# Kernel tuning notes

Measured on AMD Instinct MI355X. Metric: run time of the kernel, lower is better.

Reference implementation:

```python
import jax, jax.numpy as jnp
import numpy as np

# Config matching init_kwargs: in_dim=128, kernal_sz=8 -> d=16 units per side
D = 16      # grid of units per side
K = 8       # kernel (patch) size
C = 3       # input channels
OUT = 1000  # out_chnls (codebook size per unit)
B = 64      # batch
BETA = 10.0 # softmax temperature (init arg beta)


def setup_inputs() -> dict:
    key = jax.random.key(0)
    k1, k2 = jax.random.split(key)
    x = jax.random.normal(k1, (B, C, D * K, D * K), dtype=jnp.float32)
    # Independent weights per (w,h) unit: [d, d, out_chnls, k*k*C]
    W = jax.random.normal(k2, (D, D, OUT, C * K * K), dtype=jnp.float32) * 0.02
    return {"x": x, "W": W}


def reference(x, W):
    Bn = x.shape[0]
    P = C * K * K
    # Patch extraction matching x[:, :, k*w:k*w+k, k*h:k*h+k].reshape(B, -1)
    # (channel-major flatten of each non-overlapping k x k patch)
    patches = (
        x.reshape(Bn, C, D, K, D, K)          # (b, c, w, kh, h, kw)
         .transpose(0, 2, 4, 1, 3, 5)          # (b, w, h, c, kh, kw)
         .reshape(Bn, D, D, P)
    )
    # infer: per-unit linear infer_step -> a[b, o, w, h]
    a = jnp.einsum('bwhp,whop->bowh', patches, W)
    # per-patch competitive softmax selection over the unit's channels
    z = jax.nn.softmax(BETA * a, axis=1)
    # predict: decode code back to patch via W^T, scatter back into image
    pred = jnp.einsum('bowh,whop->bwhp', z, W)
    p = (
        pred.reshape(Bn, D, D, C, K, K)        # (b, w, h, c, kh, kw)
            .transpose(0, 3, 1, 4, 2, 5)        # (b, c, w, kh, h, kw)
            .reshape(Bn, C, D * K, D * K)
    )
    return p
```

## Files before the change

### kernel.cpp

```cpp
#include <hip/hip_runtime.h>


#define Dd 16
#define OUTC 1000
#define Pp 192
#define Bb 64
#define OT 64
#define NT 16
#define THREADS 512
#define BETA 10.0f

typedef __attribute__((ext_vector_type(8))) short short8;
typedef __attribute__((ext_vector_type(4))) float f32x4;

#define MFMA(a, b, c) __builtin_amdgcn_mfma_f32_16x16x32_bf16((a), (b), (c), 0, 0, 0)

__device__ __forceinline__ unsigned f2bf(float f) {
  unsigned u = __float_as_uint(f);
  return (u + 0x7fffu + ((u >> 16) & 1u)) >> 16;
}

__device__ __forceinline__ int paddr(int b, int p) {
  return b * 384 + ((((p) >> 3) ^ (b & 7)) << 4) + ((p) & 7) * 2;
}
__device__ __forceinline__ int waddr(int o, int p) {
  int f = (o & 7) ^ ((o >> 3) & 3);
  return o * 384 + ((((p) >> 3) ^ f) << 4) + ((p) & 7) * 2;
}
__device__ __forceinline__ int eaddr(int b, int o) {
  return b * 128 + ((((o) >> 3) ^ (b & 7)) << 4) + ((o) & 7) * 2;
}

__device__ __forceinline__ void cvt_hilo4(const float4 v, uint2& hi2, uint2& lo2) {
  unsigned h0 = f2bf(v.x), h1 = f2bf(v.y), h2 = f2bf(v.z), h3 = f2bf(v.w);
  float l0 = v.x - __uint_as_float(h0 << 16);
  float l1 = v.y - __uint_as_float(h1 << 16);
  float l2 = v.z - __uint_as_float(h2 << 16);
  float l3 = v.w - __uint_as_float(h3 << 16);
  unsigned g0 = f2bf(l0), g1 = f2bf(l1), g2 = f2bf(l2), g3 = f2bf(l3);
  hi2 = make_uint2(h0 | (h1 << 16), h2 | (h3 << 16));
  lo2 = make_uint2(g0 | (g1 << 16), g2 | (g3 << 16));
}

__global__ __launch_bounds__(THREADS, 2)
void local_layer_mfma(const float* __restrict__ x,
                      const float* __restrict__ W,
                      float* __restrict__ out) {
  __shared__ unsigned short pH[Bb * Pp];
  __shared__ unsigned short pL[Bb * Pp];
  __shared__ unsigned short wHs[OT * Pp];
  __shared__ unsigned short wLs[OT * Pp];
  __shared__ unsigned short eSs[Bb * OT];
  __shared__ float lS[Bb];

  char* pHc = (char*)pH; char* pLc = (char*)pL;
  char* wHc = (char*)wHs; char* wLc = (char*)wLs;
  char* eSc = (char*)eSs;

  const int u = blockIdx.x, uw = u >> 4, uh = u & 15;
  const int tid = threadIdx.x;
  const int wv = tid >> 6, lane = tid & 63;
  const int lr = lane & 15, lg = lane >> 4;
  const int mw = wv & 1;
  const int ow = wv >> 1;
  const int bB = 32 * mw;

  const float* Wu = W + (size_t)u * (OUTC * Pp);

  if (tid < Bb) lS[tid] = 0.f;

  float4 R[6];
#pragma unroll
  for (int k = 0; k < 6; ++k) {
    int i4 = tid + THREADS * k;
    int o = i4 / 48, p = (i4 % 48) * 4;
    R[k] = *reinterpret_cast<const float4*>(Wu + o * Pp + p);
  }

  for (int i4 = tid; i4 < Bb * 48; i4 += THREADS) {
    int b = i4 / 48, q = i4 - b * 48, p = q * 4;
    int c = p >> 6, kh = (p >> 3) & 7, kw = p & 7;
    float4 v = *reinterpret_cast<const float4*>(
        x + ((size_t)((b * 3 + c) * 128 + uw * 8 + kh) * 128 + uh * 8 + kw));
    uint2 hi2, lo2;
    cvt_hilo4(v, hi2, lo2);
    *reinterpret_cast<uint2*>(pHc + paddr(b, p)) = hi2;
    *reinterpret_cast<uint2*>(pLc + paddr(b, p)) = lo2;
  }

#pragma unroll
  for (int k = 0; k < 6; ++k) {
    int i4 = tid + THREADS * k;
    int o = i4 / 48, p = (i4 % 48) * 4;
    uint2 hi2, lo2;
    cvt_hilo4(R[k], hi2, lo2);
    *reinterpret_cast<uint2*>(wHc + waddr(o, p)) = hi2;
    *reinterpret_cast<uint2*>(wLc + waddr(o, p)) = lo2;
  }
  __syncthreads();

  short8 pa_h[2][6], pa_l[2][6];
#pragma unroll
  for (int h = 0; h < 2; ++h)
#pragma unroll
    for (int ks = 0; ks < 6; ++ks) {
      pa_h[h][ks] = *reinterpret_cast<const short8*>(pHc + paddr(bB + 16 * h + lr, 32 * ks + 8 * lg));
      pa_l[h][ks] = *reinterpret_cast<const short8*>(pLc + paddr(bB + 16 * h + lr, 32 * ks + 8 * lg));
    }

  f32x4 pacc[2][3];
#pragma unroll
  for (int h = 0; h < 2; ++h)
#pragma unroll
    for (int f = 0; f < 3; ++f) pacc[h][f] = (f32x4){0.f, 0.f, 0.f, 0.f};
  float lPartA[2][4] = {{0.f, 0.f, 0.f, 0.f}, {0.f, 0.f, 0.f, 0.f}};

  for (int t = 0; t < NT; ++t) {
    if (t + 1 < NT) {
#pragma unroll
      for (int k = 0; k < 6; ++k) {
        int i4 = tid + THREADS * k;
        int o = i4 / 48, p = (i4 % 48) * 4;
        int o_g = (t + 1) * OT + o;
        R[k] = (o_g < OUTC)
                   ? *reinterpret_cast<const float4*>(Wu + (size_t)o_g * Pp + p)
                   : make_float4(0.f, 0.f, 0.f, 0.f);
      }
    }

    f32x4 acc[2] = {(f32x4){0.f, 0.f, 0.f, 0.f}, (f32x4){0.f, 0.f, 0.f, 0.f}};
#pragma unroll
    for (int ks = 0; ks < 6; ++ks) {
      short8 wbh = *reinterpret_cast<const short8*>(wHc + waddr(16 * ow + lr, 32 * ks + 8 * lg));
      short8 wbl = *reinterpret_cast<const short8*>(wLc + waddr(16 * ow + lr, 32 * ks + 8 * lg));
#pragma unroll
      for (int h = 0; h < 2; ++h) {
        acc[h] = MFMA(pa_h[h][ks], wbh, acc[h]);
        acc[h] = MFMA(pa_h[h][ks], wbl, acc[h]);
        acc[h] = MFMA(pa_l[h][ks], wbh, acc[h]);
      }
    }

    {
      const int o_g = t * OT + 16 * ow + lr;
      const bool valid = (o_g < OUTC);
#pragma unroll
      for (int h = 0; h < 2; ++h)
#pragma unroll
        for (int j = 0; j < 4; ++j) {
          float e = valid ? __expf(BETA * acc[h][j]) : 0.f;
          lPartA[h][j] += e;
          *reinterpret_cast<unsigned short*>(
              eSc + eaddr(bB + 16 * h + 4 * lg + j, 16 * ow + lr)) =
              (unsigned short)f2bf(e);
        }
    }
    __syncthreads();

    short8 ea[2][2];
#pragma unroll
    for (int h = 0; h < 2; ++h)
#pragma unroll
      for (int ks2 = 0; ks2 < 2; ++ks2)
        ea[h][ks2] = *reinterpret_cast<const short8*>(
            eSc + eaddr(bB + 16 * h + lr, 32 * ks2 + 8 * lg));

#pragma unroll
    for (int f = 0; f < 3; ++f) {
      const int p = 48 * ow + 16 * f + lr;
#pragma unroll
      for (int ks2 = 0; ks2 < 2; ++ks2) {
        short8 wb;
#pragma unroll
        for (int e8 = 0; e8 < 8; ++e8)
          wb[e8] = *reinterpret_cast<const short*>(
              wHc + waddr(32 * ks2 + 8 * lg + e8, p));
#pragma unroll
        for (int h = 0; h < 2; ++h)
          pacc[h][f] = MFMA(ea[h][ks2], wb, pacc[h][f]);
      }
    }
    __syncthreads();

    if (t + 1 < NT) {
#pragma unroll
      for (int k = 0; k < 6; ++k) {
        int i4 = tid + THREADS * k;
        int o = i4 / 48, p = (i4 % 48) * 4;
        uint2 hi2, lo2;
        cvt_hilo4(R[k], hi2, lo2);
        *reinterpret_cast<uint2*>(wHc + waddr(o, p)) = hi2;
        *reinterpret_cast<uint2*>(wLc + waddr(o, p)) = lo2;
      }
      __syncthreads();
    }
  }

#pragma unroll
  for (int h = 0; h < 2; ++h)
#pragma unroll
    for (int j = 0; j < 4; ++j) {
      float v = lPartA[h][j];
      v += __shfl_xor(v, 1, 16);
      v += __shfl_xor(v, 2, 16);
      v += __shfl_xor(v, 4, 16);
      v += __shfl_xor(v, 8, 16);
      if (lr == 0) atomicAdd(&lS[bB + 16 * h + 4 * lg + j], v);
    }
  __syncthreads();

#pragma unroll
  for (int h = 0; h < 2; ++h) {
    float inv[4];
#pragma unroll
    for (int j = 0; j < 4; ++j) inv[j] = 1.f / lS[bB + 16 * h + 4 * lg + j];
#pragma unroll
    for (int f = 0; f < 3; ++f) {
      const int p = 48 * ow + 16 * f + lr;
      const int c = p >> 6, kh = (p >> 3) & 7, kw = p & 7;
#pragma unroll
      for (int j = 0; j < 4; ++j) {
        const int b = bB + 16 * h + 4 * lg + j;
        out[((size_t)((b * 3 + c) * 128 + uw * 8 + kh)) * 128 + uh * 8 + kw] =
            pacc[h][f][j] * inv[j];
      }
    }
  }
}

extern "C" void kernel_launch(void* const* d_in, const int* in_sizes, int n_in,
                              void* d_out, int out_size, void* d_ws, size_t ws_size,
                              hipStream_t stream) {
  const float* x = (const float*)d_in[0];
  const float* W = (const float*)d_in[1];
  float* out = (float*)d_out;
  hipLaunchKernelGGL(local_layer_mfma, dim3(Dd * Dd), dim3(THREADS), 0, stream,
                     x, W, out);
}
```

Baseline: 292.5 us.

## Double block threads to sixteen waves and double-buffer weight tiles in LDS

Raises the block to 1024 threads so each wave computes 16 batch rows instead of 32, halving per-wave register state and fetching three float4 of W per thread per tile instead of six. The weight tile is now double-buffered in LDS, so the next tile is converted into the other buffer and one barrier per iteration is removed. Low-half patch fragments are now reread from LDS each iteration instead of being kept in registers. In exchange, LDS use grows to about 150KB per block and the B-operand weight fragments are read by twice as many waves.

```diff
diff --git a/kernel.cpp b/kernel.cpp
--- a/kernel.cpp
+++ b/kernel.cpp
@@ -7,7 +7,7 @@
 #define Bb 64
 #define OT 64
 #define NT 16
-#define THREADS 512
+#define THREADS 1024
 #define BETA 10.0f
 
 typedef __attribute__((ext_vector_type(8))) short short8;
@@ -42,43 +42,44 @@
   lo2 = make_uint2(g0 | (g1 << 16), g2 | (g3 << 16));
 }
 
-__global__ __launch_bounds__(THREADS, 2)
-void local_layer_mfma(const float* __restrict__ x,
-                      const float* __restrict__ W,
-                      float* __restrict__ out) {
+__global__ __launch_bounds__(THREADS, 4)
+void local_layer_mfma2(const float* __restrict__ x,
+                       const float* __restrict__ W,
+                       float* __restrict__ out) {
   __shared__ unsigned short pH[Bb * Pp];
   __shared__ unsigned short pL[Bb * Pp];
-  __shared__ unsigned short wHs[OT * Pp];
-  __shared__ unsigned short wLs[OT * Pp];
+  __shared__ unsigned short wH2[2][OT * Pp];
+  __shared__ unsigned short wL2[2][OT * Pp];
   __shared__ unsigned short eSs[Bb * OT];
   __shared__ float lS[Bb];
 
   char* pHc = (char*)pH; char* pLc = (char*)pL;
-  char* wHc = (char*)wHs; char* wLc = (char*)wLs;
   char* eSc = (char*)eSs;
 
   const int u = blockIdx.x, uw = u >> 4, uh = u & 15;
   const int tid = threadIdx.x;
   const int wv = tid >> 6, lane = tid & 63;
   const int lr = lane & 15, lg = lane >> 4;
-  const int mw = wv & 1;
-  const int ow = wv >> 1;
-  const int bB = 32 * mw;
+  const int mq = wv & 3;
+  const int ow = wv >> 2;
+  const int bB = 16 * mq;
 
   const float* Wu = W + (size_t)u * (OUTC * Pp);
 
   if (tid < Bb) lS[tid] = 0.f;
 
-  float4 R[6];
-#pragma unroll
-  for (int k = 0; k < 6; ++k) {
+  float4 R[3];
+#pragma unroll
+  for (int k = 0; k < 3; ++k) {
     int i4 = tid + THREADS * k;
     int o = i4 / 48, p = (i4 % 48) * 4;
     R[k] = *reinterpret_cast<const float4*>(Wu + o * Pp + p);
   }
 
-  for (int i4 = tid; i4 < Bb * 48; i4 += THREADS) {
-    int b = i4 / 48, q = i4 - b * 48, p = q * 4;
+#pragma unroll
+  for (int k = 0; k < 3; ++k) {
+    int i4 = tid + THREADS * k;
+    int b = i4 / 48, q = i4 % 48, p = q * 4;
     int c = p >> 6, kh = (p >> 3) & 7, kw = p & 7;
     float4 v = *reinterpret_cast<const float4*>(
         x + ((size_t)((b * 3 + c) * 128 + uw * 8 + kh) * 128 + uh * 8 + kw));
@@ -88,37 +89,38 @@
     *reinterpret_cast<uint2*>(pLc + paddr(b, p)) = lo2;
   }
 
-#pragma unroll
-  for (int k = 0; k < 6; ++k) {
-    int i4 = tid + THREADS * k;
-    int o = i4 / 48, p = (i4 % 48) * 4;
-    uint2 hi2, lo2;
-    cvt_hilo4(R[k], hi2, lo2);
-    *reinterpret_cast<uint2*>(wHc + waddr(o, p)) = hi2;
-    *reinterpret_cast<uint2*>(wLc + waddr(o, p)) = lo2;
+  {
+    char* wHc = (char*)wH2[0];
+    char* wLc = (char*)wL2[0];
+#pragma unroll
+    for (int k = 0; k < 3; ++k) {
+      int i4 = tid + THREADS * k;
+      int o = i4 / 48, p = (i4 % 48) * 4;
+      uint2 hi2, lo2;
+      cvt_hilo4(R[k], hi2, lo2);
+      *reinterpret_cast<uint2*>(wHc + waddr(o, p)) = hi2;
+      *reinterpret_cast<uint2*>(wLc + waddr(o, p)) = lo2;
+    }
   }
   __syncthreads();
 
-  short8 pa_h[2][6], pa_l[2][6];
-#pragma unroll
-  for (int h = 0; h < 2; ++h)
-#pragma unroll
-    for (int ks = 0; ks < 6; ++ks) {
-      pa_h[h][ks] = *reinterpret_cast<const short8*>(pHc + paddr(bB + 16 * h + lr, 32 * ks + 8 * lg));
-      pa_l[h][ks] = *reinterpret_cast<const short8*>(pLc + paddr(bB + 16 * h + lr, 32 * ks + 8 * lg));
-    }
-
-  f32x4 pacc[2][3];
-#pragma unroll
-  for (int h = 0; h < 2; ++h)
-#pragma unroll
-    for (int f = 0; f < 3; ++f) pacc[h][f] = (f32x4){0.f, 0.f, 0.f, 0.f};
-  float lPartA[2][4] = {{0.f, 0.f, 0.f, 0.f}, {0.f, 0.f, 0.f, 0.f}};
+  short8 pa_h[6];
+#pragma unroll
+  for (int ks = 0; ks < 6; ++ks)
+    pa_h[ks] = *reinterpret_cast<const short8*>(pHc + paddr(bB + lr, 32 * ks + 8 * lg));
+
+  f32x4 pacc[3];
+#pragma unroll
+  for (int f = 0; f < 3; ++f) pacc[f] = (f32x4){0.f, 0.f, 0.f, 0.f};
+  float lPart[4] = {0.f, 0.f, 0.f, 0.f};
 
   for (int t = 0; t < NT; ++t) {
+    char* wHc = (char*)wH2[t & 1];
+    char* wLc = (char*)wL2[t & 1];
+
     if (t + 1 < NT) {
 #pragma unroll
-      for (int k = 0; k < 6; ++k) {
+      for (int k = 0; k < 3; ++k) {
         int i4 = tid + THREADS * k;
         int o = i4 / 48, p = (i4 % 48) * 4;
         int o_g = (t + 1) * OT + o;
@@ -128,42 +130,36 @@
       }
     }
 
-    f32x4 acc[2] = {(f32x4){0.f, 0.f, 0.f, 0.f}, (f32x4){0.f, 0.f, 0.f, 0.f}};
+    f32x4 acc = (f32x4){0.f, 0.f, 0.f, 0.f};
 #pragma unroll
     for (int ks = 0; ks < 6; ++ks) {
-      short8 wbh = *reinterpret_cast<const short8*>(wHc + waddr(16 * ow + lr, 32 * ks + 8 * lg));
-      short8 wbl = *reinterpret_cast<const short8*>(wLc + waddr(16 * ow + lr, 32 * ks + 8 * lg));
-#pragma unroll
-      for (int h = 0; h < 2; ++h) {
-        acc[h] = MFMA(pa_h[h][ks], wbh, acc[h]);
-        acc[h] = MFMA(pa_h[h][ks], wbl, acc[h]);
-        acc[h] = MFMA(pa_l[h][ks], wbh, acc[h]);
-      }
+      const int ko = 32 * ks + 8 * lg;
+      short8 wbh = *reinterpret_cast<const short8*>(wHc + waddr(16 * ow + lr, ko));
+      short8 wbl = *reinterpret_cast<const short8*>(wLc + waddr(16 * ow + lr, ko));
+      short8 pal = *reinterpret_cast<const short8*>(pLc + paddr(bB + lr, ko));
+      acc = MFMA(pa_h[ks], wbh, acc);
+      acc = MFMA(pa_h[ks], wbl, acc);
+      acc = MFMA(pal, wbh, acc);
     }
 
     {
       const int o_g = t * OT + 16 * ow + lr;
       const bool valid = (o_g < OUTC);
 #pragma unroll
-      for (int h = 0; h < 2; ++h)
-#pragma unroll
-        for (int j = 0; j < 4; ++j) {
-          float e = valid ? __expf(BETA * acc[h][j]) : 0.f;
-          lPartA[h][j] += e;
-          *reinterpret_cast<unsigned short*>(
-              eSc + eaddr(bB + 16 * h + 4 * lg + j, 16 * ow + lr)) =
-              (unsigned short)f2bf(e);
-        }
+      for (int j = 0; j < 4; ++j) {
+        float e = valid ? __expf(BETA * acc[j]) : 0.f;
+        lPart[j] += e;
+        *reinterpret_cast<unsigned short*>(
+            eSc + eaddr(bB + 4 * lg + j, 16 * ow + lr)) = (unsigned short)f2bf(e);
+      }
     }
     __syncthreads();
 
-    short8 ea[2][2];
-#pragma unroll
-    for (int h = 0; h < 2; ++h)
-#pragma unroll
-      for (int ks2 = 0; ks2 < 2; ++ks2)
-        ea[h][ks2] = *reinterpret_cast<const short8*>(
-            eSc + eaddr(bB + 16 * h + lr, 32 * ks2 + 8 * lg));
+    short8 ea[2];
+#pragma unroll
+    for (int ks2 = 0; ks2 < 2; ++ks2)
+      ea[ks2] = *reinterpret_cast<const short8*>(
+          eSc + eaddr(bB + lr, 32 * ks2 + 8 * lg));
 
 #pragma unroll
     for (int f = 0; f < 3; ++f) {
@@ -175,55 +171,49 @@
         for (int e8 = 0; e8 < 8; ++e8)
           wb[e8] = *reinterpret_cast<const short*>(
               wHc + waddr(32 * ks2 + 8 * lg + e8, p));
-#pragma unroll
-        for (int h = 0; h < 2; ++h)
-          pacc[h][f] = MFMA(ea[h][ks2], wb, pacc[h][f]);
-      }
-    }
-    __syncthreads();
+        pacc[f] = MFMA(ea[ks2], wb, pacc[f]);
+      }
+    }
 
     if (t + 1 < NT) {
-#pragma unroll
-      for (int k = 0; k < 6; ++k) {
+      char* nH = (char*)wH2[(t + 1) & 1];
+      char* nL = (char*)wL2[(t + 1) & 1];
+#pragma unroll
+      for (int k = 0; k < 3; ++k) {
         int i4 = tid + THREADS * k;
         int o = i4 / 48, p = (i4 % 48) * 4;
         uint2 hi2, lo2;
         cvt_hilo4(R[k], hi2, lo2);
-        *reinterpret_cast<uint2*>(wHc + waddr(o, p)) = hi2;
-        *reinterpret_cast<uint2*>(wLc + waddr(o, p)) = lo2;
-      }
-      __syncthreads();
-    }
-  }
-
-#pragma unroll
-  for (int h = 0; h < 2; ++h)
+        *reinterpret_cast<uint2*>(nH + waddr(o, p)) = hi2;
+        *reinterpret_cast<uint2*>(nL + waddr(o, p)) = lo2;
+      }
+    }
+    __syncthreads();
+  }
+
+#pragma unroll
+  for (int j = 0; j < 4; ++j) {
+    float v = lPart[j];
+    v += __shfl_xor(v, 1, 16);
+    v += __shfl_xor(v, 2, 16);
+    v += __shfl_xor(v, 4, 16);
+    v += __shfl_xor(v, 8, 16);
+    if (lr == 0) atomicAdd(&lS[bB + 4 * lg + j], v);
+  }
+  __syncthreads();
+
+  float inv[4];
+#pragma unroll
+  for (int j = 0; j < 4; ++j) inv[j] = 1.f / lS[bB + 4 * lg + j];
+#pragma unroll
+  for (int f = 0; f < 3; ++f) {
+    const int p = 48 * ow + 16 * f + lr;
+    const int c = p >> 6, kh = (p >> 3) & 7, kw = p & 7;
 #pragma unroll
     for (int j = 0; j < 4; ++j) {
-      float v = lPartA[h][j];
-      v += __shfl_xor(v, 1, 16);
-      v += __shfl_xor(v, 2, 16);
-      v += __shfl_xor(v, 4, 16);
-      v += __shfl_xor(v, 8, 16);
-      if (lr == 0) atomicAdd(&lS[bB + 16 * h + 4 * lg + j], v);
-    }
-  __syncthreads();
-
-#pragma unroll
-  for (int h = 0; h < 2; ++h) {
-    float inv[4];
-#pragma unroll
-    for (int j = 0; j < 4; ++j) inv[j] = 1.f / lS[bB + 16 * h + 4 * lg + j];
-#pragma unroll
-    for (int f = 0; f < 3; ++f) {
-      const int p = 48 * ow + 16 * f + lr;
-      const int c = p >> 6, kh = (p >> 3) & 7, kw = p & 7;
-#pragma unroll
-      for (int j = 0; j < 4; ++j) {
-        const int b = bB + 16 * h + 4 * lg + j;
-        out[((size_t)((b * 3 + c) * 128 + uw * 8 + kh)) * 128 + uh * 8 + kw] =
-            pacc[h][f][j] * inv[j];
-      }
+      const int b = bB + 4 * lg + j;
+      out[((size_t)((b * 3 + c) * 128 + uw * 8 + kh)) * 128 + uh * 8 + kw] =
+          pacc[f][j] * inv[j];
     }
   }
 }
@@ -234,6 +224,6 @@
   const float* x = (const float*)d_in[0];
   const float* W = (const float*)d_in[1];
   float* out = (float*)d_out;
-  hipLaunchKernelGGL(local_layer_mfma, dim3(Dd * Dd), dim3(THREADS), 0, stream,
+  hipLaunchKernelGGL(local_layer_mfma2, dim3(Dd * Dd), dim3(THREADS), 0, stream,
                      x, W, out);
 }
```

Result: slower. 310.7 us (+6.3%).
